# Performance work log

Hardware: AMD Instinct MI355X
Metric: run time of the kernel (lower is better)

Reference implementation:

```python
import jax, jax.numpy as jnp
import numpy as np

N, E, DIN, HID, HEADS = 50000, 400000, 256, 64, 4
EPS_BN = 1e-5

def setup_inputs() -> dict:
    key = jax.random.key(0)
    ks = jax.random.split(key, 12)
    inp = {}
    inp['x'] = jax.random.normal(ks[0], (N, DIN), dtype=jnp.float32)
    inp['edge_index'] = jax.random.randint(ks[1], (2, E), 0, N, dtype=jnp.int64)
    s = 1.0 / np.sqrt(DIN)
    inp['W1'] = jax.random.uniform(ks[2], (DIN, HEADS * HID), jnp.float32, -s, s)
    inp['a_src1'] = jax.random.normal(ks[3], (HEADS, HID), dtype=jnp.float32) * 0.1
    inp['a_dst1'] = jax.random.normal(ks[4], (HEADS, HID), dtype=jnp.float32) * 0.1
    inp['b1'] = jnp.zeros((HEADS * HID,), jnp.float32)
    inp['bn1_w'] = jnp.ones((HEADS * HID,), jnp.float32)
    inp['bn1_b'] = jnp.zeros((HEADS * HID,), jnp.float32)
    inp['bn1_m'] = jnp.zeros((HEADS * HID,), jnp.float32)
    inp['bn1_v'] = jnp.ones((HEADS * HID,), jnp.float32)
    s2 = 1.0 / np.sqrt(HEADS * HID)
    inp['W2'] = jax.random.uniform(ks[5], (HEADS * HID, HID), jnp.float32, -s2, s2)
    inp['a_src2'] = jax.random.normal(ks[6], (1, HID), dtype=jnp.float32) * 0.1
    inp['a_dst2'] = jax.random.normal(ks[7], (1, HID), dtype=jnp.float32) * 0.1
    inp['b2'] = jnp.zeros((HID,), jnp.float32)
    inp['bn2_w'] = jnp.ones((HID,), jnp.float32)
    inp['bn2_b'] = jnp.zeros((HID,), jnp.float32)
    inp['bn2_m'] = jnp.zeros((HID,), jnp.float32)
    inp['bn2_v'] = jnp.ones((HID,), jnp.float32)
    sr = 1.0 / np.sqrt(HID)
    inp['Wr'] = jax.random.uniform(ks[8], (HID, 1), jnp.float32, -sr, sr)
    inp['br'] = jnp.zeros((1,), jnp.float32)
    inp['Wc'] = jax.random.uniform(ks[9], (HID, 1), jnp.float32, -sr, sr)
    inp['bc'] = jnp.zeros((1,), jnp.float32)
    return inp

def gat_layer(x, src, dst, W, a_src, a_dst, bias, concat):
    # x: [N, Fin] -> h: [N, H, D]
    H, D = a_src.shape
    h = (x @ W).reshape(-1, H, D)
    alpha_s = jnp.sum(h * a_src[None], axis=-1)  # [N, H]
    alpha_d = jnp.sum(h * a_dst[None], axis=-1)
    e = jax.nn.leaky_relu(alpha_s[src] + alpha_d[dst], 0.2)  # [Et, H]
    m = jax.ops.segment_max(e, dst, num_segments=N)
    m = jnp.where(jnp.isfinite(m), m, 0.0)
    ex = jnp.exp(e - m[dst])
    denom = jax.ops.segment_sum(ex, dst, num_segments=N)
    alpha = ex / (denom[dst] + 1e-16)  # segment softmax over incoming edges
    msg = h[src] * alpha[:, :, None]  # [Et, H, D]
    out = jax.ops.segment_sum(msg, dst, num_segments=N)  # [N, H, D]
    out = out.reshape(N, H * D) if concat else out.mean(axis=1)
    return out + bias

def batchnorm(x, w, b, mean, var):
    return (x - mean) * jax.lax.rsqrt(var + EPS_BN) * w + b

def reference(x, edge_index, W1, a_src1, a_dst1, b1, bn1_w, bn1_b, bn1_m, bn1_v,
              W2, a_src2, a_dst2, b2, bn2_w, bn2_b, bn2_m, bn2_v, Wr, br, Wc, bc):
    # add self loops (PyG GATConv default)
    loops = jnp.arange(N, dtype=edge_index.dtype)
    src = jnp.concatenate([edge_index[0], loops])
    dst = jnp.concatenate([edge_index[1], loops])
    h = gat_layer(x, src, dst, W1, a_src1, a_dst1, b1, concat=True)
    h = jax.nn.elu(batchnorm(h, bn1_w, bn1_b, bn1_m, bn1_v))
    h = gat_layer(h, src, dst, W2, a_src2, a_dst2, b2, concat=False)
    h = jax.nn.elu(batchnorm(h, bn2_w, bn2_b, bn2_m, bn2_v))
    reg = h @ Wr + br
    clf = jax.nn.sigmoid(h @ Wc + bc)
    return reg, clf
```

## Files before the change

### kernel.cpp

```cpp
#include <hip/hip_runtime.h>
#include <math.h>


typedef unsigned short ushort_t;
typedef __attribute__((ext_vector_type(8))) unsigned short ushort8;
typedef __attribute__((ext_vector_type(4))) unsigned short ushort4v;
typedef __attribute__((ext_vector_type(8))) short short8;
typedef __attribute__((ext_vector_type(4))) float f32x4;

__device__ __forceinline__ ushort_t f2bf(float f) {
  unsigned u = __float_as_uint(f);
  unsigned r = u + 0x7fffu + ((u >> 16) & 1u);
  return (ushort_t)(r >> 16);
}
__device__ __forceinline__ float bf2f(ushort_t h) {
  return __uint_as_float((unsigned)h << 16);
}
__device__ __forceinline__ float leaky02(float x) { return x >= 0.f ? x : 0.2f * x; }

__device__ __forceinline__ float wave_sum(float v) {
#pragma unroll
  for (int o = 1; o < 64; o <<= 1) v += __shfl_xor(v, o, 64);
  return v;
}
__device__ __forceinline__ int wave_incl_scan(int v, int lane) {
#pragma unroll
  for (int off = 1; off < 64; off <<= 1) {
    int t = __shfl_up(v, off, 64);
    if (lane >= off) v += t;
  }
  return v;
}

__device__ __forceinline__ void gld_lds16(const ushort_t* g, ushort_t* l) {
  __builtin_amdgcn_global_load_lds(
      (const __attribute__((address_space(1))) unsigned int*)g,
      (__attribute__((address_space(3))) unsigned int*)l, 16, 0, 0);
}

__global__ void zero_two(int* a, int* b, int n) {
  int i = blockIdx.x * blockDim.x + threadIdx.x;
  if (i < n) { a[i] = 0; b[i] = 0; }
}

__global__ void hist_kernel(const int* __restrict__ dst, int* __restrict__ counts, int E) {
  int e = blockIdx.x * blockDim.x + threadIdx.x;
  if (e < E) atomicAdd(&counts[dst[e]], 1);
}

__global__ __launch_bounds__(256) void scan_chunks_kernel(const int* __restrict__ counts,
                                                          int* __restrict__ offsets,
                                                          int* __restrict__ partials, int N) {
  __shared__ int ws[4];
  int tid = threadIdx.x, lane = tid & 63, wv = tid >> 6;
  int i = blockIdx.x * 256 + tid;
  int v = (i < N) ? counts[i] : 0;
  int incl = wave_incl_scan(v, lane);
  if (lane == 63) ws[wv] = incl;
  __syncthreads();
  int wbase = 0;
  for (int k = 0; k < wv; ++k) wbase += ws[k];
  if (i < N) offsets[i] = wbase + incl - v;
  if (tid == 255) partials[blockIdx.x] = wbase + incl;
}

__global__ __launch_bounds__(256) void scan_partials_kernel(const int* __restrict__ partials,
                                                            int* __restrict__ pprefix, int nb) {
  __shared__ int ws[4];
  int tid = threadIdx.x, lane = tid & 63, wv = tid >> 6;
  int v = (tid < nb) ? partials[tid] : 0;
  int incl = wave_incl_scan(v, lane);
  if (lane == 63) ws[wv] = incl;
  __syncthreads();
  int wbase = 0;
  for (int k = 0; k < wv; ++k) wbase += ws[k];
  if (tid < nb) pprefix[tid] = wbase + incl - v;
  if (tid == 255) pprefix[nb] = wbase + incl;
}

__global__ void add_base_kernel(int* __restrict__ offsets, const int* __restrict__ pprefix,
                                int N, int nb) {
  int i = blockIdx.x * 256 + threadIdx.x;
  if (i < N) offsets[i] += pprefix[blockIdx.x];
  if (i == 0) offsets[N] = pprefix[nb];
}

__global__ void scatter_kernel(const int* __restrict__ src, const int* __restrict__ dst,
                               const int* __restrict__ offsets, int* __restrict__ cursor,
                               int* __restrict__ csr_src, int E) {
  int e = blockIdx.x * blockDim.x + threadIdx.x;
  if (e < E) {
    int d = dst[e];
    int p = atomicAdd(&cursor[d], 1);
    csr_src[offsets[d] + p] = src[e];
  }
}

__global__ void cast_bf16_kernel(const float* __restrict__ in, ushort_t* __restrict__ out, int n4) {
  int i = blockIdx.x * blockDim.x + threadIdx.x;
  if (i < n4) {
    float4 v = ((const float4*)in)[i];
    ushort4 o;
    o.x = f2bf(v.x); o.y = f2bf(v.y); o.z = f2bf(v.z); o.w = f2bf(v.w);
    ((ushort4*)out)[i] = o;
  }
}

__global__ void prep_weights_kernel(const float* __restrict__ W1, const float* __restrict__ W2,
                                    ushort_t* __restrict__ W1t, ushort_t* __restrict__ W2t) {
  int i = blockIdx.x * 256 + threadIdx.x;
  if (i < 256 * 256) {
    int k = i >> 8, n2 = i & 255;
    W1t[n2 * 256 + k] = f2bf(W1[i]);
  } else {
    int j = i - 256 * 256;
    if (j < 256 * 64) {
      int k = j >> 6, n2 = j & 63;
      W2t[n2 * 256 + k] = f2bf(W2[j]);
    }
  }
}

template <int WM>
__global__ __launch_bounds__(WM * 64) void mfma_gemm_fused(
    const ushort_t* __restrict__ A, const ushort_t* __restrict__ Bt,
    ushort_t* __restrict__ C, const float* __restrict__ avs, const float* __restrict__ avd,
    float* __restrict__ as_out, float* __restrict__ ad_out, int M, int Nt, int K, int H) {
  constexpr int BM = WM * 32;
  constexpr int NB = 4 / WM;
  __shared__ ushort_t As[BM * 32];
  __shared__ ushort_t Bs[64 * 32];
  const int t = threadIdx.x;
  const int w = t >> 6, l = t & 63;
  const int m0 = blockIdx.y * BM;
  const int n0 = blockIdx.x * 64;
  const int head = n0 >> 6;

  f32x4 zero4 = {0.f, 0.f, 0.f, 0.f};
  f32x4 acc[2][4];
#pragma unroll
  for (int i = 0; i < 2; ++i)
#pragma unroll
    for (int j = 0; j < 4; ++j) acc[i][j] = zero4;

  const int scol = (l & 3) * 8;
  const ushort_t* Aga[2];
  ushort_t* Asl[2];
#pragma unroll
  for (int a = 0; a < 2; ++a) {
    int r = (a * WM + w) * 16 + (l >> 2);
    int gr = min(m0 + r, M - 1);
    Aga[a] = A + (size_t)gr * K + scol;
    Asl[a] = &As[(a * WM + w) * 512];
  }
  const ushort_t* Bgb[NB];
  ushort_t* Bsl[NB];
#pragma unroll
  for (int b = 0; b < NB; ++b) {
    int r = (b * WM + w) * 16 + (l >> 2);
    Bgb[b] = Bt + (size_t)(n0 + r) * K + scol;
    Bsl[b] = &Bs[(b * WM + w) * 512];
  }

  for (int k0 = 0; k0 < K; k0 += 32) {
    __syncthreads();
#pragma unroll
    for (int a = 0; a < 2; ++a) gld_lds16(Aga[a] + k0, Asl[a]);
#pragma unroll
    for (int b = 0; b < NB; ++b) gld_lds16(Bgb[b] + k0, Bsl[b]);
    __syncthreads();
    const int kq = (l >> 4) * 8;
    short8 af[2], bfr[4];
#pragma unroll
    for (int i = 0; i < 2; ++i)
      af[i] = *(const short8*)&As[(w * 32 + i * 16 + (l & 15)) * 32 + kq];
#pragma unroll
    for (int j = 0; j < 4; ++j)
      bfr[j] = *(const short8*)&Bs[(j * 16 + (l & 15)) * 32 + kq];
#pragma unroll
    for (int i = 0; i < 2; ++i)
#pragma unroll
      for (int j = 0; j < 4; ++j)
        acc[i][j] = __builtin_amdgcn_mfma_f32_16x16x32_bf16(af[i], bfr[j], acc[i][j], 0, 0, 0);
  }

  const int rbase = m0 + w * 32 + (l >> 4) * 4;
  const int cbase = n0 + (l & 15);
#pragma unroll
  for (int i = 0; i < 2; ++i)
#pragma unroll
    for (int j = 0; j < 4; ++j)
#pragma unroll
      for (int r = 0; r < 4; ++r) {
        int row = rbase + i * 16 + r;
        if (row < M) C[(size_t)row * Nt + cbase + j * 16] = f2bf(acc[i][j][r]);
      }

  float asw[4], adw[4];
#pragma unroll
  for (int j = 0; j < 4; ++j) {
    asw[j] = avs[head * 64 + (l & 15) + j * 16];
    adw[j] = avd[head * 64 + (l & 15) + j * 16];
  }
#pragma unroll
  for (int i = 0; i < 2; ++i)
#pragma unroll
    for (int r = 0; r < 4; ++r) {
      float s_ = acc[i][0][r] * asw[0] + acc[i][1][r] * asw[1] +
                 acc[i][2][r] * asw[2] + acc[i][3][r] * asw[3];
      float d_ = acc[i][0][r] * adw[0] + acc[i][1][r] * adw[1] +
                 acc[i][2][r] * adw[2] + acc[i][3][r] * adw[3];
#pragma unroll
      for (int o = 1; o < 16; o <<= 1) {
        s_ += __shfl_xor(s_, o, 64);
        d_ += __shfl_xor(d_, o, 64);
      }
      if ((l & 15) == 0) {
        int row = rbase + i * 16 + r;
        if (row < M) {
          as_out[(size_t)row * H + head] = s_;
          ad_out[(size_t)row * H + head] = d_;
        }
      }
    }
}

__global__ __launch_bounds__(256) void agg1_kernel(
    const ushort_t* __restrict__ h1, const int* __restrict__ offsets,
    const int* __restrict__ csr, const float* __restrict__ as1,
    const float* __restrict__ ad1, const float* __restrict__ b1,
    const float* __restrict__ bnw, const float* __restrict__ bnb,
    const float* __restrict__ bnm, const float* __restrict__ bnv,
    ushort_t* __restrict__ out, int N) {
  int n = blockIdx.x * 4 + (threadIdx.x >> 6);
  int l = threadIdx.x & 63;
  if (n >= N) return;
  const int g = l >> 5, ll = l & 31;
  const int hh = ll >> 3;
  int off = offsets[n], deg = offsets[n + 1] - off;
  float4 ad4 = *(const float4*)&ad1[n * 4];
  float adv[4] = {ad4.x, ad4.y, ad4.z, ad4.w};
  float acc[8] = {0, 0, 0, 0, 0, 0, 0, 0};
  float ds[4] = {0, 0, 0, 0};

  for (int base = 0; base < deg; base += 64) {
    bool inb = base + l < deg;
    int sj = inb ? csr[off + base + l] : 0;
    float w0 = 0.f, w1 = 0.f, w2 = 0.f, w3 = 0.f;
    if (inb) {
      float4 a4 = *(const float4*)&as1[sj * 4];
      w0 = __expf(leaky02(a4.x + adv[0]));
      w1 = __expf(leaky02(a4.y + adv[1]));
      w2 = __expf(leaky02(a4.z + adv[2]));
      w3 = __expf(leaky02(a4.w + adv[3]));
    }
    ds[0] += w0; ds[1] += w1; ds[2] += w2; ds[3] += w3;
    int cnt = min(64, deg - base);
    int sl0 = min(g, cnt - 1);
    int s_c = __shfl(sj, sl0, 64);
    float a0 = __shfl(w0, sl0, 64), a1 = __shfl(w1, sl0, 64),
          a2 = __shfl(w2, sl0, 64), a3 = __shfl(w3, sl0, 64);
    float lo = (hh & 1) ? a1 : a0, hi = (hh & 1) ? a3 : a2;
    float w_c = (hh & 2) ? hi : lo;
    if (g >= cnt) w_c = 0.f;
    ushort8 hv_c = *(const ushort8*)&h1[(size_t)s_c * 256 + ll * 8];
    for (int j = 2; j < cnt; j += 2) {
      int sl1 = min(j + g, cnt - 1);
      int s_n = __shfl(sj, sl1, 64);
      float b0 = __shfl(w0, sl1, 64), b1_ = __shfl(w1, sl1, 64),
            b2_ = __shfl(w2, sl1, 64), b3 = __shfl(w3, sl1, 64);
      float nlo = (hh & 1) ? b1_ : b0, nhi = (hh & 1) ? b3 : b2_;
      float w_n = (hh & 2) ? nhi : nlo;
      if (j + g >= cnt) w_n = 0.f;
      ushort8 hv_n = *(const ushort8*)&h1[(size_t)s_n * 256 + ll * 8];
#pragma unroll
      for (int k = 0; k < 8; ++k) acc[k] = fmaf(w_c, bf2f(hv_c[k]), acc[k]);
      w_c = w_n; hv_c = hv_n;
    }
#pragma unroll
    for (int k = 0; k < 8; ++k) acc[k] = fmaf(w_c, bf2f(hv_c[k]), acc[k]);
  }
#pragma unroll
  for (int k = 0; k < 8; ++k) acc[k] += __shfl_xor(acc[k], 32, 64);
  float den[4];
#pragma unroll
  for (int h = 0; h < 4; ++h) den[h] = wave_sum(ds[h]);
  float4 asn4 = *(const float4*)&as1[n * 4];
  float asn[4] = {asn4.x, asn4.y, asn4.z, asn4.w};
  float wsf[4];
#pragma unroll
  for (int h = 0; h < 4; ++h) {
    wsf[h] = __expf(leaky02(asn[h] + adv[h]));
    den[h] += wsf[h];
  }
  ushort8 hvn = *(const ushort8*)&h1[(size_t)n * 256 + ll * 8];
  float wsh = wsf[hh];
#pragma unroll
  for (int k = 0; k < 8; ++k) acc[k] = fmaf(wsh, bf2f(hvn[k]), acc[k]);
  float inv_den = 1.f / (den[hh] + 1e-16f);
  int c0 = ll * 8 + g * 4;
  float4 bb = *(const float4*)&b1[c0];
  float4 bw = *(const float4*)&bnw[c0];
  float4 bbb = *(const float4*)&bnb[c0];
  float4 bm = *(const float4*)&bnm[c0];
  float4 bv = *(const float4*)&bnv[c0];
  float bbf[4] = {bb.x, bb.y, bb.z, bb.w};
  float bwf[4] = {bw.x, bw.y, bw.z, bw.w};
  float bbbf[4] = {bbb.x, bbb.y, bbb.z, bbb.w};
  float bmf[4] = {bm.x, bm.y, bm.z, bm.w};
  float bvf[4] = {bv.x, bv.y, bv.z, bv.w};
  ushort4v o4;
#pragma unroll
  for (int q = 0; q < 4; ++q) {
    float o = acc[g * 4 + q] * inv_den + bbf[q];
    o = (o - bmf[q]) * rsqrtf(bvf[q] + 1e-5f) * bwf[q] + bbbf[q];
    o = o > 0.f ? o : expm1f(o);
    o4[q] = f2bf(o);
  }
  *(ushort4v*)&out[(size_t)n * 256 + c0] = o4;
}

__global__ __launch_bounds__(256) void agg2_kernel(
    const ushort_t* __restrict__ h2, const int* __restrict__ offsets,
    const int* __restrict__ csr, const float* __restrict__ as2,
    const float* __restrict__ ad2, const float* __restrict__ b2,
    const float* __restrict__ bnw, const float* __restrict__ bnb,
    const float* __restrict__ bnm, const float* __restrict__ bnv,
    const float* __restrict__ Wr, const float* __restrict__ br,
    const float* __restrict__ Wc, const float* __restrict__ bc,
    float* __restrict__ out_reg, float* __restrict__ out_clf, int N) {
  int n = blockIdx.x * 4 + (threadIdx.x >> 6);
  int l = threadIdx.x & 63;
  if (n >= N) return;
  const int g = l >> 4, ll = l & 15;
  int off = offsets[n], deg = offsets[n + 1] - off;
  float adv = ad2[n];
  float acc[4] = {0, 0, 0, 0};
  float ds = 0.f;

  for (int base = 0; base < deg; base += 64) {
    bool inb = base + l < deg;
    int sj = inb ? csr[off + base + l] : 0;
    float w = inb ? __expf(leaky02(as2[sj] + adv)) : 0.f;
    ds += w;
    int cnt = min(64, deg - base);
    int sl0 = min(g, cnt - 1);
    int s_c = __shfl(sj, sl0, 64);
    float w_c = __shfl(w, sl0, 64);
    if (g >= cnt) w_c = 0.f;
    ushort4v hv_c = *(const ushort4v*)&h2[(size_t)s_c * 64 + ll * 4];
    for (int j = 4; j < cnt; j += 4) {
      int sl1 = min(j + g, cnt - 1);
      int s_n = __shfl(sj, sl1, 64);
      float w_n = __shfl(w, sl1, 64);
      if (j + g >= cnt) w_n = 0.f;
      ushort4v hv_n = *(const ushort4v*)&h2[(size_t)s_n * 64 + ll * 4];
#pragma unroll
      for (int k = 0; k < 4; ++k) acc[k] = fmaf(w_c, bf2f(hv_c[k]), acc[k]);
      w_c = w_n; hv_c = hv_n;
    }
#pragma unroll
    for (int k = 0; k < 4; ++k) acc[k] = fmaf(w_c, bf2f(hv_c[k]), acc[k]);
  }
#pragma unroll
  for (int k = 0; k < 4; ++k) {
    acc[k] += __shfl_xor(acc[k], 16, 64);
    acc[k] += __shfl_xor(acc[k], 32, 64);
  }
  float den = wave_sum(ds);
  float ws = __expf(leaky02(as2[n] + adv));
  den += ws;
  ushort4v hvn = *(const ushort4v*)&h2[(size_t)n * 64 + ll * 4];
#pragma unroll
  for (int k = 0; k < 4; ++k) acc[k] = fmaf(ws, bf2f(hvn[k]), acc[k]);

  float inv_den = 1.f / (den + 1e-16f);
  int c0 = ll * 4;
  float4 bb = *(const float4*)&b2[c0];
  float4 bw = *(const float4*)&bnw[c0];
  float4 bbb = *(const float4*)&bnb[c0];
  float4 bm = *(const float4*)&bnm[c0];
  float4 bv = *(const float4*)&bnv[c0];
  float4 wr = *(const float4*)&Wr[c0];
  float4 wc = *(const float4*)&Wc[c0];
  float bbf[4] = {bb.x, bb.y, bb.z, bb.w};
  float bwf[4] = {bw.x, bw.y, bw.z, bw.w};
  float bbbf[4] = {bbb.x, bbb.y, bbb.z, bbb.w};
  float bmf[4] = {bm.x, bm.y, bm.z, bm.w};
  float bvf[4] = {bv.x, bv.y, bv.z, bv.w};
  float wrf[4] = {wr.x, wr.y, wr.z, wr.w};
  float wcf[4] = {wc.x, wc.y, wc.z, wc.w};
  float rs = 0.f, cs = 0.f;
#pragma unroll
  for (int q = 0; q < 4; ++q) {
    float o = acc[q] * inv_den + bbf[q];
    o = (o - bmf[q]) * rsqrtf(bvf[q] + 1e-5f) * bwf[q] + bbbf[q];
    o = o > 0.f ? o : expm1f(o);
    rs = fmaf(o, wrf[q], rs);
    cs = fmaf(o, wcf[q], cs);
  }
  float rsum = wave_sum(rs) * 0.25f;
  float csum = wave_sum(cs) * 0.25f;
  if (l == 0) {
    out_reg[n] = rsum + br[0];
    float z = csum + bc[0];
    out_clf[n] = 1.f / (1.f + __expf(-z));
  }
}

extern "C" void kernel_launch(void* const* d_in, const int* in_sizes, int n_in,
                              void* d_out, int out_size, void* d_ws, size_t ws_size,
                              hipStream_t stream) {
  const float* x      = (const float*)d_in[0];
  const int*   ei     = (const int*)d_in[1];
  const float* W1     = (const float*)d_in[2];
  const float* a_src1 = (const float*)d_in[3];
  const float* a_dst1 = (const float*)d_in[4];
  const float* b1     = (const float*)d_in[5];
  const float* bn1w   = (const float*)d_in[6];
  const float* bn1b   = (const float*)d_in[7];
  const float* bn1m   = (const float*)d_in[8];
  const float* bn1v   = (const float*)d_in[9];
  const float* W2     = (const float*)d_in[10];
  const float* a_src2 = (const float*)d_in[11];
  const float* a_dst2 = (const float*)d_in[12];
  const float* b2     = (const float*)d_in[13];
  const float* bn2w   = (const float*)d_in[14];
  const float* bn2b   = (const float*)d_in[15];
  const float* bn2m   = (const float*)d_in[16];
  const float* bn2v   = (const float*)d_in[17];
  const float* Wr     = (const float*)d_in[18];
  const float* br     = (const float*)d_in[19];
  const float* Wc     = (const float*)d_in[20];
  const float* bc     = (const float*)d_in[21];

  const int N = in_sizes[0] / 256;
  const int E = in_sizes[1] / 2;
  const int* srcv = ei;
  const int* dstv = ei + E;

  char* w = (char*)d_ws;
  auto alloc = [&](size_t bytes) {
    char* p = w;
    w += (bytes + 255) & ~(size_t)255;
    return p;
  };
  const int nb = (N + 255) / 256;
  int* counts    = (int*)alloc((size_t)N * 4);
  int* cursor    = (int*)alloc((size_t)N * 4);
  int* offsets   = (int*)alloc((size_t)(N + 1) * 4);
  int* partials  = (int*)alloc((size_t)nb * 4);
  int* pprefix   = (int*)alloc((size_t)(nb + 1) * 4);
  int* csr_src   = (int*)alloc((size_t)E * 4);
  float* as1     = (float*)alloc((size_t)N * 4 * 4);
  float* ad1     = (float*)alloc((size_t)N * 4 * 4);
  float* as2     = (float*)alloc((size_t)N * 4);
  float* ad2     = (float*)alloc((size_t)N * 4);
  ushort_t* xb   = (ushort_t*)alloc((size_t)N * 256 * 2);
  ushort_t* W1t  = (ushort_t*)alloc((size_t)256 * 256 * 2);
  ushort_t* W2t  = (ushort_t*)alloc((size_t)64 * 256 * 2);
  ushort_t* h1b  = (ushort_t*)alloc((size_t)N * 256 * 2);
  ushort_t* h1a  = (ushort_t*)alloc((size_t)N * 256 * 2);
  ushort_t* h2b  = (ushort_t*)alloc((size_t)N * 64 * 2);

  float* out_reg = (float*)d_out;

  zero_two<<<(N + 255) / 256, 256, 0, stream>>>(counts, cursor, N);
  hist_kernel<<<(E + 255) / 256, 256, 0, stream>>>(dstv, counts, E);
  scan_chunks_kernel<<<nb, 256, 0, stream>>>(counts, offsets, partials, N);
  scan_partials_kernel<<<1, 256, 0, stream>>>(partials, pprefix, nb);
  add_base_kernel<<<nb, 256, 0, stream>>>(offsets, pprefix, N, nb);
  scatter_kernel<<<(E + 255) / 256, 256, 0, stream>>>(srcv, dstv, offsets, cursor, csr_src, E);

  cast_bf16_kernel<<<(N * 256 / 4 + 255) / 256, 256, 0, stream>>>(x, xb, N * 256 / 4);
  prep_weights_kernel<<<(256 * 256 + 256 * 64 + 255) / 256, 256, 0, stream>>>(W1, W2, W1t, W2t);

  const int nwb = (N + 3) / 4;

  dim3 g1(4, (N + 127) / 128);
  mfma_gemm_fused<4><<<g1, 256, 0, stream>>>(xb, W1t, h1b, a_src1, a_dst1, as1, ad1,
                                             N, 256, 256, 4);
  agg1_kernel<<<nwb, 256, 0, stream>>>(h1b, offsets, csr_src, as1, ad1, b1,
                                       bn1w, bn1b, bn1m, bn1v, h1a, N);

  dim3 g2(1, (N + 63) / 64);
  mfma_gemm_fused<2><<<g2, 128, 0, stream>>>(h1a, W2t, h2b, a_src2, a_dst2, as2, ad2,
                                             N, 64, 256, 1);
  agg2_kernel<<<nwb, 256, 0, stream>>>(h2b, offsets, csr_src, as2, ad2, b2,
                                       bn2w, bn2b, bn2m, bn2v, Wr, br, Wc, bc,
                                       out_reg, out_reg + N, N);
}
```

Before: 290.2 us.

## Fuse x cast into GEMM, precompute edge weights, merge prep kernels

```diff
diff --git a/kernel.cpp b/kernel.cpp
--- a/kernel.cpp
+++ b/kernel.cpp
@@ -38,9 +38,26 @@
       (__attribute__((address_space(3))) unsigned int*)l, 16, 0, 0);
 }
 
-__global__ void zero_two(int* a, int* b, int n) {
-  int i = blockIdx.x * blockDim.x + threadIdx.x;
-  if (i < n) { a[i] = 0; b[i] = 0; }
+__global__ void prep_kernel(int* __restrict__ counts, int* __restrict__ cursor,
+                            const float* __restrict__ W1, const float* __restrict__ W2,
+                            ushort_t* __restrict__ W1t, ushort_t* __restrict__ W2t, int N) {
+  int i = blockIdx.x * 256 + threadIdx.x;
+  if (i < N) {
+    counts[i] = 0;
+    cursor[i] = 0;
+    return;
+  }
+  int j = i - N;
+  if (j < 256 * 256) {
+    int k = j >> 8, n2 = j & 255;
+    W1t[n2 * 256 + k] = f2bf(W1[j]);
+    return;
+  }
+  j -= 256 * 256;
+  if (j < 256 * 64) {
+    int k = j >> 6, n2 = j & 63;
+    W2t[n2 * 256 + k] = f2bf(W2[j]);
+  }
 }
 
 __global__ void hist_kernel(const int* __restrict__ dst, int* __restrict__ counts, int E) {
@@ -87,43 +104,59 @@
 
 __global__ void scatter_kernel(const int* __restrict__ src, const int* __restrict__ dst,
                                const int* __restrict__ offsets, int* __restrict__ cursor,
-                               int* __restrict__ csr_src, int E) {
+                               int* __restrict__ csr_src, int* __restrict__ csr_dst, int E) {
   int e = blockIdx.x * blockDim.x + threadIdx.x;
   if (e < E) {
     int d = dst[e];
     int p = atomicAdd(&cursor[d], 1);
-    csr_src[offsets[d] + p] = src[e];
-  }
-}
-
-__global__ void cast_bf16_kernel(const float* __restrict__ in, ushort_t* __restrict__ out, int n4) {
-  int i = blockIdx.x * blockDim.x + threadIdx.x;
-  if (i < n4) {
-    float4 v = ((const float4*)in)[i];
-    ushort4 o;
-    o.x = f2bf(v.x); o.y = f2bf(v.y); o.z = f2bf(v.z); o.w = f2bf(v.w);
-    ((ushort4*)out)[i] = o;
-  }
-}
-
-__global__ void prep_weights_kernel(const float* __restrict__ W1, const float* __restrict__ W2,
-                                    ushort_t* __restrict__ W1t, ushort_t* __restrict__ W2t) {
-  int i = blockIdx.x * 256 + threadIdx.x;
-  if (i < 256 * 256) {
-    int k = i >> 8, n2 = i & 255;
-    W1t[n2 * 256 + k] = f2bf(W1[i]);
-  } else {
-    int j = i - 256 * 256;
-    if (j < 256 * 64) {
-      int k = j >> 6, n2 = j & 63;
-      W2t[n2 * 256 + k] = f2bf(W2[j]);
-    }
-  }
-}
-
-template <int WM>
+    int pos = offsets[d] + p;
+    csr_src[pos] = src[e];
+    csr_dst[pos] = d;
+  }
+}
+
+__global__ void edge_weights1(const int* __restrict__ csr_src, const int* __restrict__ csr_dst,
+                              const float* __restrict__ as1, const float* __restrict__ ad1,
+                              float* __restrict__ we, float* __restrict__ wself, int E, int N) {
+  int t = blockIdx.x * 256 + threadIdx.x;
+  if (t < E) {
+    int s = csr_src[t], d = csr_dst[t];
+    float4 a = *(const float4*)&as1[s * 4];
+    float4 b = *(const float4*)&ad1[d * 4];
+    float4 o;
+    o.x = __expf(leaky02(a.x + b.x));
+    o.y = __expf(leaky02(a.y + b.y));
+    o.z = __expf(leaky02(a.z + b.z));
+    o.w = __expf(leaky02(a.w + b.w));
+    *(float4*)&we[(size_t)t * 4] = o;
+  } else if (t < E + N) {
+    int n = t - E;
+    float4 a = *(const float4*)&as1[n * 4];
+    float4 b = *(const float4*)&ad1[n * 4];
+    float4 o;
+    o.x = __expf(leaky02(a.x + b.x));
+    o.y = __expf(leaky02(a.y + b.y));
+    o.z = __expf(leaky02(a.z + b.z));
+    o.w = __expf(leaky02(a.w + b.w));
+    *(float4*)&wself[n * 4] = o;
+  }
+}
+
+__global__ void edge_weights2(const int* __restrict__ csr_src, const int* __restrict__ csr_dst,
+                              const float* __restrict__ as2, const float* __restrict__ ad2,
+                              float* __restrict__ we, float* __restrict__ wself, int E, int N) {
+  int t = blockIdx.x * 256 + threadIdx.x;
+  if (t < E) {
+    we[t] = __expf(leaky02(as2[csr_src[t]] + ad2[csr_dst[t]]));
+  } else if (t < E + N) {
+    int n = t - E;
+    wself[n] = __expf(leaky02(as2[n] + ad2[n]));
+  }
+}
+
+template <int WM, bool CASTA>
 __global__ __launch_bounds__(WM * 64) void mfma_gemm_fused(
-    const ushort_t* __restrict__ A, const ushort_t* __restrict__ Bt,
+    const void* __restrict__ Ain, const ushort_t* __restrict__ Bt,
     ushort_t* __restrict__ C, const float* __restrict__ avs, const float* __restrict__ avd,
     float* __restrict__ as_out, float* __restrict__ ad_out, int M, int Nt, int K, int H) {
   constexpr int BM = WM * 32;
@@ -144,15 +177,6 @@
     for (int j = 0; j < 4; ++j) acc[i][j] = zero4;
 
   const int scol = (l & 3) * 8;
-  const ushort_t* Aga[2];
-  ushort_t* Asl[2];
-#pragma unroll
-  for (int a = 0; a < 2; ++a) {
-    int r = (a * WM + w) * 16 + (l >> 2);
-    int gr = min(m0 + r, M - 1);
-    Aga[a] = A + (size_t)gr * K + scol;
-    Asl[a] = &As[(a * WM + w) * 512];
-  }
   const ushort_t* Bgb[NB];
   ushort_t* Bsl[NB];
 #pragma unroll
@@ -161,14 +185,49 @@
     Bgb[b] = Bt + (size_t)(n0 + r) * K + scol;
     Bsl[b] = &Bs[(b * WM + w) * 512];
   }
+  const ushort_t* Aga[2];
+  ushort_t* Asl[2];
+  const float* Axg = nullptr;
+  ushort_t* AsWc = nullptr;
+  if (CASTA) {
+    int ar = t >> 1, ac = (t & 1) * 16;
+    Axg = (const float*)Ain + (size_t)min(m0 + ar, M - 1) * K + ac;
+    AsWc = &As[ar * 32 + ac];
+  } else {
+#pragma unroll
+    for (int a = 0; a < 2; ++a) {
+      int r = (a * WM + w) * 16 + (l >> 2);
+      int gr = min(m0 + r, M - 1);
+      Aga[a] = (const ushort_t*)Ain + (size_t)gr * K + scol;
+      Asl[a] = &As[(a * WM + w) * 512];
+    }
+  }
 
   for (int k0 = 0; k0 < K; k0 += 32) {
-    __syncthreads();
-#pragma unroll
-    for (int a = 0; a < 2; ++a) gld_lds16(Aga[a] + k0, Asl[a]);
-#pragma unroll
-    for (int b = 0; b < NB; ++b) gld_lds16(Bgb[b] + k0, Bsl[b]);
-    __syncthreads();
+    if (CASTA) {
+      float4 f0 = *(const float4*)(Axg + k0);
+      float4 f1 = *(const float4*)(Axg + k0 + 4);
+      float4 f2 = *(const float4*)(Axg + k0 + 8);
+      float4 f3 = *(const float4*)(Axg + k0 + 12);
+      __syncthreads();
+#pragma unroll
+      for (int b = 0; b < NB; ++b) gld_lds16(Bgb[b] + k0, Bsl[b]);
+      ushort8 u0, u1;
+      u0[0] = f2bf(f0.x); u0[1] = f2bf(f0.y); u0[2] = f2bf(f0.z); u0[3] = f2bf(f0.w);
+      u0[4] = f2bf(f1.x); u0[5] = f2bf(f1.y); u0[6] = f2bf(f1.z); u0[7] = f2bf(f1.w);
+      u1[0] = f2bf(f2.x); u1[1] = f2bf(f2.y); u1[2] = f2bf(f2.z); u1[3] = f2bf(f2.w);
+      u1[4] = f2bf(f3.x); u1[5] = f2bf(f3.y); u1[6] = f2bf(f3.z); u1[7] = f2bf(f3.w);
+      *(ushort8*)AsWc = u0;
+      *(ushort8*)(AsWc + 8) = u1;
+      __syncthreads();
+    } else {
+      __syncthreads();
+#pragma unroll
+      for (int a = 0; a < 2; ++a) gld_lds16(Aga[a] + k0, Asl[a]);
+#pragma unroll
+      for (int b = 0; b < NB; ++b) gld_lds16(Bgb[b] + k0, Bsl[b]);
+      __syncthreads();
+    }
     const int kq = (l >> 4) * 8;
     short8 af[2], bfr[4];
 #pragma unroll
@@ -227,55 +286,49 @@
 
 __global__ __launch_bounds__(256) void agg1_kernel(
     const ushort_t* __restrict__ h1, const int* __restrict__ offsets,
-    const int* __restrict__ csr, const float* __restrict__ as1,
-    const float* __restrict__ ad1, const float* __restrict__ b1,
+    const int* __restrict__ csr, const float* __restrict__ we,
+    const float* __restrict__ wself, const float* __restrict__ b1,
     const float* __restrict__ bnw, const float* __restrict__ bnb,
     const float* __restrict__ bnm, const float* __restrict__ bnv,
     ushort_t* __restrict__ out, int N) {
   int n = blockIdx.x * 4 + (threadIdx.x >> 6);
   int l = threadIdx.x & 63;
   if (n >= N) return;
-  const int g = l >> 5, ll = l & 31;
-  const int hh = ll >> 3;
+  const int g = l >> 5, ll = l & 31, hh = ll >> 3;
   int off = offsets[n], deg = offsets[n + 1] - off;
-  float4 ad4 = *(const float4*)&ad1[n * 4];
-  float adv[4] = {ad4.x, ad4.y, ad4.z, ad4.w};
   float acc[8] = {0, 0, 0, 0, 0, 0, 0, 0};
   float ds[4] = {0, 0, 0, 0};
 
   for (int base = 0; base < deg; base += 64) {
-    bool inb = base + l < deg;
-    int sj = inb ? csr[off + base + l] : 0;
-    float w0 = 0.f, w1 = 0.f, w2 = 0.f, w3 = 0.f;
-    if (inb) {
-      float4 a4 = *(const float4*)&as1[sj * 4];
-      w0 = __expf(leaky02(a4.x + adv[0]));
-      w1 = __expf(leaky02(a4.y + adv[1]));
-      w2 = __expf(leaky02(a4.z + adv[2]));
-      w3 = __expf(leaky02(a4.w + adv[3]));
-    }
-    ds[0] += w0; ds[1] += w1; ds[2] += w2; ds[3] += w3;
     int cnt = min(64, deg - base);
-    int sl0 = min(g, cnt - 1);
-    int s_c = __shfl(sj, sl0, 64);
-    float a0 = __shfl(w0, sl0, 64), a1 = __shfl(w1, sl0, 64),
-          a2 = __shfl(w2, sl0, 64), a3 = __shfl(w3, sl0, 64);
-    float lo = (hh & 1) ? a1 : a0, hi = (hh & 1) ? a3 : a2;
-    float w_c = (hh & 2) ? hi : lo;
+    if (l < cnt) {
+      float4 w4 = *(const float4*)&we[(size_t)(off + base + l) * 4];
+      ds[0] += w4.x; ds[1] += w4.y; ds[2] += w4.z; ds[3] += w4.w;
+    }
+    int e0 = off + base + min(g, cnt - 1);
+    int s_c = csr[e0];
+    float w_c = we[(size_t)e0 * 4 + hh];
     if (g >= cnt) w_c = 0.f;
     ushort8 hv_c = *(const ushort8*)&h1[(size_t)s_c * 256 + ll * 8];
+    int s_n = 0; float w_n = 0.f;
+    if (cnt > 2) {
+      int e1 = off + base + min(2 + g, cnt - 1);
+      s_n = csr[e1];
+      w_n = we[(size_t)e1 * 4 + hh];
+      if (2 + g >= cnt) w_n = 0.f;
+    }
     for (int j = 2; j < cnt; j += 2) {
-      int sl1 = min(j + g, cnt - 1);
-      int s_n = __shfl(sj, sl1, 64);
-      float b0 = __shfl(w0, sl1, 64), b1_ = __shfl(w1, sl1, 64),
-            b2_ = __shfl(w2, sl1, 64), b3 = __shfl(w3, sl1, 64);
-      float nlo = (hh & 1) ? b1_ : b0, nhi = (hh & 1) ? b3 : b2_;
-      float w_n = (hh & 2) ? nhi : nlo;
-      if (j + g >= cnt) w_n = 0.f;
+      int s_f = 0; float w_f = 0.f;
+      if (j + 2 < cnt) {
+        int ef = off + base + min(j + 2 + g, cnt - 1);
+        s_f = csr[ef];
+        w_f = we[(size_t)ef * 4 + hh];
+        if (j + 2 + g >= cnt) w_f = 0.f;
+      }
       ushort8 hv_n = *(const ushort8*)&h1[(size_t)s_n * 256 + ll * 8];
 #pragma unroll
       for (int k = 0; k < 8; ++k) acc[k] = fmaf(w_c, bf2f(hv_c[k]), acc[k]);
-      w_c = w_n; hv_c = hv_n;
+      s_c = s_n; w_c = w_n; hv_c = hv_n; s_n = s_f; w_n = w_f;
     }
 #pragma unroll
     for (int k = 0; k < 8; ++k) acc[k] = fmaf(w_c, bf2f(hv_c[k]), acc[k]);
@@ -285,14 +338,10 @@
   float den[4];
 #pragma unroll
   for (int h = 0; h < 4; ++h) den[h] = wave_sum(ds[h]);
-  float4 asn4 = *(const float4*)&as1[n * 4];
-  float asn[4] = {asn4.x, asn4.y, asn4.z, asn4.w};
-  float wsf[4];
-#pragma unroll
-  for (int h = 0; h < 4; ++h) {
-    wsf[h] = __expf(leaky02(asn[h] + adv[h]));
-    den[h] += wsf[h];
-  }
+  float4 ws4 = *(const float4*)&wself[n * 4];
+  float wsf[4] = {ws4.x, ws4.y, ws4.z, ws4.w};
+#pragma unroll
+  for (int h = 0; h < 4; ++h) den[h] += wsf[h];
   ushort8 hvn = *(const ushort8*)&h1[(size_t)n * 256 + ll * 8];
   float wsh = wsf[hh];
 #pragma unroll
@@ -322,8 +371,8 @@
 
 __global__ __launch_bounds__(256) void agg2_kernel(
     const ushort_t* __restrict__ h2, const int* __restrict__ offsets,
-    const int* __restrict__ csr, const float* __restrict__ as2,
-    const float* __restrict__ ad2, const float* __restrict__ b2,
+    const int* __restrict__ csr, const float* __restrict__ we,
+    const float* __restrict__ wself, const float* __restrict__ b2,
     const float* __restrict__ bnw, const float* __restrict__ bnb,
     const float* __restrict__ bnm, const float* __restrict__ bnv,
     const float* __restrict__ Wr, const float* __restrict__ br,
@@ -334,30 +383,36 @@
   if (n >= N) return;
   const int g = l >> 4, ll = l & 15;
   int off = offsets[n], deg = offsets[n + 1] - off;
-  float adv = ad2[n];
   float acc[4] = {0, 0, 0, 0};
   float ds = 0.f;
 
   for (int base = 0; base < deg; base += 64) {
-    bool inb = base + l < deg;
-    int sj = inb ? csr[off + base + l] : 0;
-    float w = inb ? __expf(leaky02(as2[sj] + adv)) : 0.f;
-    ds += w;
     int cnt = min(64, deg - base);
-    int sl0 = min(g, cnt - 1);
-    int s_c = __shfl(sj, sl0, 64);
-    float w_c = __shfl(w, sl0, 64);
+    if (l < cnt) ds += we[off + base + l];
+    int e0 = off + base + min(g, cnt - 1);
+    int s_c = csr[e0];
+    float w_c = we[e0];
     if (g >= cnt) w_c = 0.f;
     ushort4v hv_c = *(const ushort4v*)&h2[(size_t)s_c * 64 + ll * 4];
+    int s_n = 0; float w_n = 0.f;
+    if (cnt > 4) {
+      int e1 = off + base + min(4 + g, cnt - 1);
+      s_n = csr[e1];
+      w_n = we[e1];
+      if (4 + g >= cnt) w_n = 0.f;
+    }
     for (int j = 4; j < cnt; j += 4) {
-      int sl1 = min(j + g, cnt - 1);
-      int s_n = __shfl(sj, sl1, 64);
-      float w_n = __shfl(w, sl1, 64);
-      if (j + g >= cnt) w_n = 0.f;
+      int s_f = 0; float w_f = 0.f;
+      if (j + 4 < cnt) {
+        int ef = off + base + min(j + 4 + g, cnt - 1);
+        s_f = csr[ef];
+        w_f = we[ef];
+        if (j + 4 + g >= cnt) w_f = 0.f;
+      }
       ushort4v hv_n = *(const ushort4v*)&h2[(size_t)s_n * 64 + ll * 4];
 #pragma unroll
       for (int k = 0; k < 4; ++k) acc[k] = fmaf(w_c, bf2f(hv_c[k]), acc[k]);
-      w_c = w_n; hv_c = hv_n;
+      s_c = s_n; w_c = w_n; hv_c = hv_n; s_n = s_f; w_n = w_f;
     }
 #pragma unroll
     for (int k = 0; k < 4; ++k) acc[k] = fmaf(w_c, bf2f(hv_c[k]), acc[k]);
@@ -368,7 +423,7 @@
     acc[k] += __shfl_xor(acc[k], 32, 64);
   }
   float den = wave_sum(ds);
-  float ws = __expf(leaky02(as2[n] + adv));
+  float ws = wself[n];
   den += ws;
   ushort4v hvn = *(const ushort4v*)&h2[(size_t)n * 64 + ll * 4];
 #pragma unroll
@@ -452,11 +507,15 @@
   int* partials  = (int*)alloc((size_t)nb * 4);
   int* pprefix   = (int*)alloc((size_t)(nb + 1) * 4);
   int* csr_src   = (int*)alloc((size_t)E * 4);
+  int* csr_dst   = (int*)alloc((size_t)E * 4);
   float* as1     = (float*)alloc((size_t)N * 4 * 4);
   float* ad1     = (float*)alloc((size_t)N * 4 * 4);
   float* as2     = (float*)alloc((size_t)N * 4);
   float* ad2     = (float*)alloc((size_t)N * 4);
-  ushort_t* xb   = (ushort_t*)alloc((size_t)N * 256 * 2);
+  float* we1     = (float*)alloc((size_t)E * 4 * 4);
+  float* wself1  = (float*)alloc((size_t)N * 4 * 4);
+  float* we2     = (float*)alloc((size_t)E * 4);
+  float* wself2  = (float*)alloc((size_t)N * 4);
   ushort_t* W1t  = (ushort_t*)alloc((size_t)256 * 256 * 2);
   ushort_t* W2t  = (ushort_t*)alloc((size_t)64 * 256 * 2);
   ushort_t* h1b  = (ushort_t*)alloc((size_t)N * 256 * 2);
@@ -465,28 +524,31 @@
 
   float* out_reg = (float*)d_out;
 
-  zero_two<<<(N + 255) / 256, 256, 0, stream>>>(counts, cursor, N);
+  int prep_items = N + 256 * 256 + 256 * 64;
+  prep_kernel<<<(prep_items + 255) / 256, 256, 0, stream>>>(counts, cursor, W1, W2, W1t, W2t, N);
+
   hist_kernel<<<(E + 255) / 256, 256, 0, stream>>>(dstv, counts, E);
   scan_chunks_kernel<<<nb, 256, 0, stream>>>(counts, offsets, partials, N);
   scan_partials_kernel<<<1, 256, 0, stream>>>(partials, pprefix, nb);
   add_base_kernel<<<nb, 256, 0, stream>>>(offsets, pprefix, N, nb);
-  scatter_kernel<<<(E + 255) / 256, 256, 0, stream>>>(srcv, dstv, offsets, cursor, csr_src, E);
-
-  cast_bf16_kernel<<<(N * 256 / 4 + 255) / 256, 256, 0, stream>>>(x, xb, N * 256 / 4);
-  prep_weights_kernel<<<(256 * 256 + 256 * 64 + 255) / 256, 256, 0, stream>>>(W1, W2, W1t, W2t);
+  scatter_kernel<<<(E + 255) / 256, 256, 0, stream>>>(srcv, dstv, offsets, cursor,
+                                                      csr_src, csr_dst, E);
 
   const int nwb = (N + 3) / 4;
+  const int ewb = (E + N + 255) / 256;
 
   dim3 g1(4, (N + 127) / 128);
-  mfma_gemm_fused<4><<<g1, 256, 0, stream>>>(xb, W1t, h1b, a_src1, a_dst1, as1, ad1,
-                                             N, 256, 256, 4);
-  agg1_kernel<<<nwb, 256, 0, stream>>>(h1b, offsets, csr_src, as1, ad1, b1,
+  mfma_gemm_fused<4, true><<<g1, 256, 0, stream>>>(x, W1t, h1b, a_src1, a_dst1, as1, ad1,
+                                                   N, 256, 256, 4);
+  edge_weights1<<<ewb, 256, 0, stream>>>(csr_src, csr_dst, as1, ad1, we1, wself1, E, N);
+  agg1_kernel<<<nwb, 256, 0, stream>>>(h1b, offsets, csr_src, we1, wself1, b1,
                                        bn1w, bn1b, bn1m, bn1v, h1a, N);
 
   dim3 g2(1, (N + 63) / 64);
-  mfma_gemm_fused<2><<<g2, 128, 0, stream>>>(h1a, W2t, h2b, a_src2, a_dst2, as2, ad2,
-                                             N, 64, 256, 1);
-  agg2_kernel<<<nwb, 256, 0, stream>>>(h2b, offsets, csr_src, as2, ad2, b2,
+  mfma_gemm_fused<2, false><<<g2, 128, 0, stream>>>(h1a, W2t, h2b, a_src2, a_dst2, as2, ad2,
+                                                    N, 64, 256, 1);
+  edge_weights2<<<ewb, 256, 0, stream>>>(csr_src, csr_dst, as2, ad2, we2, wself2, E, N);
+  agg2_kernel<<<nwb, 256, 0, stream>>>(h2b, offsets, csr_src, we2, wself2, b2,
                                        bn2w, bn2b, bn2m, bn2v, Wr, br, Wc, bc,
                                        out_reg, out_reg + N, N);
 }
```

New measurement: 306.1 us. 5.5% more time.
